# Performance work log

Measured on AMD Instinct MI355X. Metric: run time of the kernel, lower is better.

Reference implementation:

```python
import jax, jax.numpy as jnp
import numpy as np

N_EXPERTS = 8
D_MODEL = 1024
D_FF = 4096


def setup_inputs() -> dict:
    key = jax.random.key(0)
    k_x, k_idx, k_g, k_u, k_d = jax.random.split(key, 5)
    scale_in = 1.0 / np.sqrt(D_MODEL)
    scale_ff = 1.0 / np.sqrt(D_FF)
    return {
        "x": jax.random.normal(k_x, (2, 1024, D_MODEL), dtype=jnp.float32),
        "expert_idx": jax.random.randint(k_idx, (2, 1024), 0, N_EXPERTS, dtype=jnp.int64),
        "w_gate": jax.random.normal(k_g, (N_EXPERTS, D_MODEL, D_FF), dtype=jnp.float32) * scale_in,
        "w_up": jax.random.normal(k_u, (N_EXPERTS, D_MODEL, D_FF), dtype=jnp.float32) * scale_in,
        "w_down": jax.random.normal(k_d, (N_EXPERTS, D_FF, D_MODEL), dtype=jnp.float32) * scale_ff,
    }


def reference(x, expert_idx, w_gate, w_up, w_down):
    # x: [B, S, D]; expert_idx: [B, S] in [0, N_EXPERTS)
    B, S, D = x.shape
    x_flat = x.reshape(-1, D)                  # [T, D]
    idx_flat = expert_idx.reshape(-1)          # [T]
    out = jnp.zeros_like(x_flat)
    # Faithful per-expert dispatch: each token is processed by exactly one
    # expert's SwiGLU FFN; masked scatter-back combines results.
    for e in range(N_EXPERTS):
        mask = (idx_flat == e)[:, None]        # [T, 1]
        gate = jax.nn.silu(x_flat @ w_gate[e]) # [T, F]
        up = x_flat @ w_up[e]                  # [T, F]
        y = (gate * up) @ w_down[e]            # [T, D]
        out = jnp.where(mask, y, out)
    return out.reshape(B, S, D)
```

## Files before the change

kernel.cpp:

```cpp
#include <hip/hip_runtime.h>
#include <hip/hip_bf16.h>
#include <stdint.h>

#define N_EXPERTS 8
#define D_MODEL   1024
#define D_FF      4096
#define T_TOKENS  2048
#define MT1       128
#define MAXT1     24
#define MT2       64
#define MAXT2     40
#define BK        64
#define KP        72

typedef __attribute__((ext_vector_type(8))) short bf16x8;
typedef __attribute__((ext_vector_type(4))) float f32x4;

__device__ __forceinline__ short f2bf(float f) {
    union { float f; uint32_t u; } v; v.f = f;
    uint32_t u = v.u;
    return (short)((u + 0x7fffu + ((u >> 16) & 1u)) >> 16);
}

__device__ __forceinline__ uint32_t pack2bf(float a, float b) {
    __hip_bfloat162 h = __float22bfloat162_rn(make_float2(a, b));
    return *(uint32_t*)&h;
}

template<int STRIDE>
__device__ __forceinline__ void ldw16(float v[16], const float* __restrict__ src) {
#pragma unroll
    for (int j = 0; j < 16; ++j) v[j] = src[(size_t)j * STRIDE];
}

__device__ __forceinline__ void stw16(short* dst, const float v[16]) {
    uint4 w0, w1;
    w0.x = pack2bf(v[0], v[1]);  w0.y = pack2bf(v[2], v[3]);
    w0.z = pack2bf(v[4], v[5]);  w0.w = pack2bf(v[6], v[7]);
    w1.x = pack2bf(v[8], v[9]);  w1.y = pack2bf(v[10], v[11]);
    w1.z = pack2bf(v[12], v[13]); w1.w = pack2bf(v[14], v[15]);
    *(uint4*)dst = w0;
    *(uint4*)(dst + 8) = w1;
}


__global__ void moe_route(const int* __restrict__ idx, int* __restrict__ offsets,
                          int* __restrict__ nt1p, int* __restrict__ t1_e,
                          int* __restrict__ t1_p0, int* __restrict__ t1_end,
                          int* __restrict__ nt2p, int* __restrict__ t2_e,
                          int* __restrict__ t2_p0, int* __restrict__ t2_end) {
    __shared__ int cnt[N_EXPERTS];
    int tid = threadIdx.x;
    if (tid < N_EXPERTS) cnt[tid] = 0;
    __syncthreads();
    for (int t = tid; t < T_TOKENS; t += 256) atomicAdd(&cnt[idx[t]], 1);
    __syncthreads();
    if (tid == 0) {
        int off = 0, nt1 = 0, nt2 = 0;
        for (int e = 0; e < N_EXPERTS; ++e) {
            offsets[e] = off;
            int c = cnt[e], end = off + c;
            for (int i = 0; i < c; i += MT1) { t1_e[nt1] = e; t1_p0[nt1] = off + i; t1_end[nt1] = end; ++nt1; }
            for (int i = 0; i < c; i += MT2) { t2_e[nt2] = e; t2_p0[nt2] = off + i; t2_end[nt2] = end; ++nt2; }
            off = end;
        }
        offsets[N_EXPERTS] = off;
        *nt1p = nt1;
        *nt2p = nt2;
    }
}

__global__ void moe_gather(const float* __restrict__ x, const int* __restrict__ idx,
                           const int* __restrict__ offsets, int* __restrict__ cursor,
                           int* __restrict__ tok_of_row, short* __restrict__ Xg) {
    __shared__ int sp;
    int t = blockIdx.x;
    if (threadIdx.x == 0) {
        int e = idx[t];
        int p = offsets[e] + atomicAdd(&cursor[e], 1);
        tok_of_row[p] = t;
        sp = p;
    }
    __syncthreads();
    int p = sp;
    const float4* src = (const float4*)(x + (size_t)t * D_MODEL);
    uint2* dst = (uint2*)(Xg + (size_t)p * D_MODEL);
    int i = threadIdx.x;
    float4 v = src[i];
    uint2 o;
    o.x = pack2bf(v.x, v.y);
    o.y = pack2bf(v.z, v.w);
    dst[i] = o;
}


__launch_bounds__(256)
__global__ void moe_gemm1(const float* __restrict__ wg, const float* __restrict__ wu,
                          const short* __restrict__ Xg, short* __restrict__ h,
                          const int* __restrict__ tile_e, const int* __restrict__ tile_p0,
                          const int* __restrict__ tile_end, const int* __restrict__ ntiles) {
    int ti = blockIdx.y;
    if (ti >= *ntiles) return;
    int e = tile_e[ti], p0 = tile_p0[ti], pend = tile_end[ti];
    int n0 = blockIdx.x * 64;

    __shared__ short Bg[2][64][KP];
    __shared__ short Bu[2][64][KP];

    int tid = threadIdx.x;
    int nl = tid & 63, kc = tid >> 6;
    int lane = tid & 63, w = tid >> 6;
    int col = lane & 15, quad = lane >> 4;

    const float* wgb = wg + (size_t)e * D_MODEL * D_FF + (size_t)(kc * 16) * D_FF + n0 + nl;
    const float* wub = wu + (size_t)e * D_MODEL * D_FF + (size_t)(kc * 16) * D_FF + n0 + nl;

    int row0 = p0 + w * 32 + col;      if (row0 > T_TOKENS - 1) row0 = T_TOKENS - 1;
    int row1 = row0 + 16;              if (row1 > T_TOKENS - 1) row1 = T_TOKENS - 1;
    const short* a0p = Xg + (size_t)row0 * D_MODEL + quad * 8;
    const short* a1p = Xg + (size_t)row1 * D_MODEL + quad * 8;

    f32x4 accg[2][4], accu[2][4];
#pragma unroll
    for (int m = 0; m < 2; ++m)
#pragma unroll
        for (int nf = 0; nf < 4; ++nf) {
            accg[m][nf] = (f32x4){0,0,0,0};
            accu[m][nf] = (f32x4){0,0,0,0};
        }

    {
        float g0[16], u0[16];
        ldw16<D_FF>(g0, wgb);
        ldw16<D_FF>(u0, wub);
        stw16(&Bg[0][nl][kc * 16], g0);
        stw16(&Bu[0][nl][kc * 16], u0);
    }
    __syncthreads();

    bf16x8 a00 = *(const bf16x8*)(a0p);
    bf16x8 a01 = *(const bf16x8*)(a0p + 32);
    bf16x8 a10 = *(const bf16x8*)(a1p);
    bf16x8 a11 = *(const bf16x8*)(a1p + 32);

    const int NIT = D_MODEL / BK;
    int p = 0;
#pragma unroll 1
    for (int it = 0; it < NIT; ++it) {
        int kn = (it + 1 == NIT) ? 0 : (it + 1) * BK;
        float gn[16], un[16];
        ldw16<D_FF>(gn, wgb + (size_t)kn * D_FF);
        ldw16<D_FF>(un, wub + (size_t)kn * D_FF);
        bf16x8 a00n = *(const bf16x8*)(a0p + kn);
        bf16x8 a01n = *(const bf16x8*)(a0p + kn + 32);
        bf16x8 a10n = *(const bf16x8*)(a1p + kn);
        bf16x8 a11n = *(const bf16x8*)(a1p + kn + 32);

#pragma unroll
        for (int nf = 0; nf < 4; ++nf) {
            bf16x8 bg0 = *(const bf16x8*)&Bg[p][nf * 16 + col][quad * 8];
            bf16x8 bg1 = *(const bf16x8*)&Bg[p][nf * 16 + col][32 + quad * 8];
            bf16x8 bu0 = *(const bf16x8*)&Bu[p][nf * 16 + col][quad * 8];
            bf16x8 bu1 = *(const bf16x8*)&Bu[p][nf * 16 + col][32 + quad * 8];
            accg[0][nf] = __builtin_amdgcn_mfma_f32_16x16x32_bf16(a00, bg0, accg[0][nf], 0, 0, 0);
            accg[0][nf] = __builtin_amdgcn_mfma_f32_16x16x32_bf16(a01, bg1, accg[0][nf], 0, 0, 0);
            accg[1][nf] = __builtin_amdgcn_mfma_f32_16x16x32_bf16(a10, bg0, accg[1][nf], 0, 0, 0);
            accg[1][nf] = __builtin_amdgcn_mfma_f32_16x16x32_bf16(a11, bg1, accg[1][nf], 0, 0, 0);
            accu[0][nf] = __builtin_amdgcn_mfma_f32_16x16x32_bf16(a00, bu0, accu[0][nf], 0, 0, 0);
            accu[0][nf] = __builtin_amdgcn_mfma_f32_16x16x32_bf16(a01, bu1, accu[0][nf], 0, 0, 0);
            accu[1][nf] = __builtin_amdgcn_mfma_f32_16x16x32_bf16(a10, bu0, accu[1][nf], 0, 0, 0);
            accu[1][nf] = __builtin_amdgcn_mfma_f32_16x16x32_bf16(a11, bu1, accu[1][nf], 0, 0, 0);
        }

        stw16(&Bg[p ^ 1][nl][kc * 16], gn);
        stw16(&Bu[p ^ 1][nl][kc * 16], un);
        a00 = a00n; a01 = a01n; a10 = a10n; a11 = a11n;
        __syncthreads();
        p ^= 1;
    }

#pragma unroll
    for (int m = 0; m < 2; ++m) {
#pragma unroll
        for (int r = 0; r < 4; ++r) {
            int mr = p0 + w * 32 + m * 16 + quad * 4 + r;
            if (mr < pend) {
#pragma unroll
                for (int nf = 0; nf < 4; ++nf) {
                    float gv = accg[m][nf][r], uv = accu[m][nf][r];
                    float hv = (gv / (1.f + __expf(-gv))) * uv;
                    h[(size_t)mr * D_FF + n0 + nf * 16 + col] = f2bf(hv);
                }
            }
        }
    }
}


__launch_bounds__(256)
__global__ void moe_gemm2(const float* __restrict__ wd, const short* __restrict__ h,
                          const int* __restrict__ tok_of_row, float* __restrict__ out,
                          const int* __restrict__ tile_e, const int* __restrict__ tile_p0,
                          const int* __restrict__ tile_end, const int* __restrict__ ntiles) {
    int ti = blockIdx.y;
    if (ti >= *ntiles) return;
    int e = tile_e[ti], p0 = tile_p0[ti], pend = tile_end[ti];
    int d0 = blockIdx.x * 64;

    __shared__ short Bd[2][64][KP];

    int tid = threadIdx.x;
    int nl = tid & 63, kc = tid >> 6;
    int lane = tid & 63, w = tid >> 6;
    int col = lane & 15, quad = lane >> 4;

    const float* wb = wd + (size_t)e * D_FF * D_MODEL + (size_t)(kc * 16) * D_MODEL + d0 + nl;

    int row0 = p0 + w * 16 + col;      if (row0 > T_TOKENS - 1) row0 = T_TOKENS - 1;
    const short* a0p = h + (size_t)row0 * D_FF + quad * 8;

    f32x4 acc[4];
#pragma unroll
    for (int nf = 0; nf < 4; ++nf) acc[nf] = (f32x4){0,0,0,0};

    {
        float w0[16];
        ldw16<D_MODEL>(w0, wb);
        stw16(&Bd[0][nl][kc * 16], w0);
    }
    __syncthreads();

    bf16x8 a0 = *(const bf16x8*)(a0p);
    bf16x8 a1 = *(const bf16x8*)(a0p + 32);

    const int NIT = D_FF / BK;
    int p = 0;
#pragma unroll 1
    for (int it = 0; it < NIT; ++it) {
        int kn = (it + 1 == NIT) ? 0 : (it + 1) * BK;
        float wn[16];
        ldw16<D_MODEL>(wn, wb + (size_t)kn * D_MODEL);
        bf16x8 a0n = *(const bf16x8*)(a0p + kn);
        bf16x8 a1n = *(const bf16x8*)(a0p + kn + 32);

#pragma unroll
        for (int nf = 0; nf < 4; ++nf) {
            bf16x8 b0 = *(const bf16x8*)&Bd[p][nf * 16 + col][quad * 8];
            bf16x8 b1 = *(const bf16x8*)&Bd[p][nf * 16 + col][32 + quad * 8];
            acc[nf] = __builtin_amdgcn_mfma_f32_16x16x32_bf16(a0, b0, acc[nf], 0, 0, 0);
            acc[nf] = __builtin_amdgcn_mfma_f32_16x16x32_bf16(a1, b1, acc[nf], 0, 0, 0);
        }

        stw16(&Bd[p ^ 1][nl][kc * 16], wn);
        a0 = a0n; a1 = a1n;
        __syncthreads();
        p ^= 1;
    }

#pragma unroll
    for (int r = 0; r < 4; ++r) {
        int mr = p0 + w * 16 + quad * 4 + r;
        if (mr < pend) {
            int t = tok_of_row[mr];
#pragma unroll
            for (int nf = 0; nf < 4; ++nf)
                out[(size_t)t * D_MODEL + d0 + nf * 16 + col] = acc[nf][r];
        }
    }
}


extern "C" void kernel_launch(void* const* d_in, const int* in_sizes, int n_in,
                              void* d_out, int out_size, void* d_ws, size_t ws_size,
                              hipStream_t stream) {
    (void)in_sizes; (void)n_in; (void)out_size; (void)ws_size;
    const float* x   = (const float*)d_in[0];
    const int*   idx = (const int*)d_in[1];
    const float* wg  = (const float*)d_in[2];
    const float* wu  = (const float*)d_in[3];
    const float* wd  = (const float*)d_in[4];
    float* out = (float*)d_out;

    int* ws_i       = (int*)d_ws;
    int* cursor     = ws_i;
    int* offsets    = ws_i + 8;
    int* nt1        = ws_i + 20;
    int* nt2        = ws_i + 21;
    int* t1_e       = ws_i + 32;
    int* t1_p0      = ws_i + 56;
    int* t1_end     = ws_i + 80;
    int* t2_e       = ws_i + 104;
    int* t2_p0      = ws_i + 144;
    int* t2_end     = ws_i + 184;
    int* tok_of_row = ws_i + 256;

    short* Xg = (short*)((char*)d_ws + 16384);
    short* h  = (short*)((char*)d_ws + 16384 + (size_t)T_TOKENS * D_MODEL * 2);

    hipMemsetAsync(d_ws, 0, 128, stream);
    moe_route<<<dim3(1), 256, 0, stream>>>(idx, offsets, nt1, t1_e, t1_p0, t1_end,
                                           nt2, t2_e, t2_p0, t2_end);
    moe_gather<<<dim3(T_TOKENS), 256, 0, stream>>>(x, idx, offsets, cursor, tok_of_row, Xg);
    moe_gemm1<<<dim3(D_FF / 64, MAXT1), 256, 0, stream>>>(wg, wu, Xg, h,
                                                          t1_e, t1_p0, t1_end, nt1);
    moe_gemm2<<<dim3(D_MODEL / 64, MAXT2), 256, 0, stream>>>(wd, h, tok_of_row, out,
                                                             t2_e, t2_p0, t2_end, nt2);
}
```

Before: 506.7 us.

## Enlarge expert token tiles to 256 rows and split-K down projection with atomics

Raises the per-expert M tile from 128/64 rows to 256 rows in both GEMMs, so each fp32 weight tile is streamed and converted once per 256 tokens instead of per 128 or 64. This cuts repeated weight reads. The down-projection GEMM gains a 4-way K split, which keeps enough blocks in flight. Partial results are combined with float atomics into an output zeroed by a memset. The cost is larger per-thread accumulator register use, A operands loaded directly without prefetch, atomic traffic on the output, and nondeterministic summation order.

```diff
diff --git a/kernel.cpp b/kernel.cpp
--- a/kernel.cpp
+++ b/kernel.cpp
@@ -6,12 +6,12 @@
 #define D_MODEL   1024
 #define D_FF      4096
 #define T_TOKENS  2048
-#define MT1       128
-#define MAXT1     24
-#define MT2       64
-#define MAXT2     40
+#define MT        256
+#define MAXT      16
 #define BK        64
 #define KP        72
+#define KSPLIT    4
+#define KS2       (D_FF / KSPLIT)
 
 typedef __attribute__((ext_vector_type(8))) short bf16x8;
 typedef __attribute__((ext_vector_type(4))) float f32x4;
@@ -45,10 +45,8 @@
 
 
 __global__ void moe_route(const int* __restrict__ idx, int* __restrict__ offsets,
-                          int* __restrict__ nt1p, int* __restrict__ t1_e,
-                          int* __restrict__ t1_p0, int* __restrict__ t1_end,
-                          int* __restrict__ nt2p, int* __restrict__ t2_e,
-                          int* __restrict__ t2_p0, int* __restrict__ t2_end) {
+                          int* __restrict__ ntp, int* __restrict__ t_e,
+                          int* __restrict__ t_p0, int* __restrict__ t_end) {
     __shared__ int cnt[N_EXPERTS];
     int tid = threadIdx.x;
     if (tid < N_EXPERTS) cnt[tid] = 0;
@@ -56,17 +54,15 @@
     for (int t = tid; t < T_TOKENS; t += 256) atomicAdd(&cnt[idx[t]], 1);
     __syncthreads();
     if (tid == 0) {
-        int off = 0, nt1 = 0, nt2 = 0;
+        int off = 0, nt = 0;
         for (int e = 0; e < N_EXPERTS; ++e) {
             offsets[e] = off;
             int c = cnt[e], end = off + c;
-            for (int i = 0; i < c; i += MT1) { t1_e[nt1] = e; t1_p0[nt1] = off + i; t1_end[nt1] = end; ++nt1; }
-            for (int i = 0; i < c; i += MT2) { t2_e[nt2] = e; t2_p0[nt2] = off + i; t2_end[nt2] = end; ++nt2; }
+            for (int i = 0; i < c; i += MT) { t_e[nt] = e; t_p0[nt] = off + i; t_end[nt] = end; ++nt; }
             off = end;
         }
         offsets[N_EXPERTS] = off;
-        *nt1p = nt1;
-        *nt2p = nt2;
+        *ntp = nt;
     }
 }
 
@@ -94,7 +90,7 @@
 }
 
 
-__launch_bounds__(256)
+__launch_bounds__(256, 2)
 __global__ void moe_gemm1(const float* __restrict__ wg, const float* __restrict__ wu,
                           const short* __restrict__ Xg, short* __restrict__ h,
                           const int* __restrict__ tile_e, const int* __restrict__ tile_p0,
@@ -115,14 +111,17 @@
     const float* wgb = wg + (size_t)e * D_MODEL * D_FF + (size_t)(kc * 16) * D_FF + n0 + nl;
     const float* wub = wu + (size_t)e * D_MODEL * D_FF + (size_t)(kc * 16) * D_FF + n0 + nl;
 
-    int row0 = p0 + w * 32 + col;      if (row0 > T_TOKENS - 1) row0 = T_TOKENS - 1;
-    int row1 = row0 + 16;              if (row1 > T_TOKENS - 1) row1 = T_TOKENS - 1;
-    const short* a0p = Xg + (size_t)row0 * D_MODEL + quad * 8;
-    const short* a1p = Xg + (size_t)row1 * D_MODEL + quad * 8;
-
-    f32x4 accg[2][4], accu[2][4];
-#pragma unroll
-    for (int m = 0; m < 2; ++m)
+    const short* ap[4];
+#pragma unroll
+    for (int m = 0; m < 4; ++m) {
+        int row = p0 + w * 64 + m * 16 + col;
+        if (row > T_TOKENS - 1) row = T_TOKENS - 1;
+        ap[m] = Xg + (size_t)row * D_MODEL + quad * 8;
+    }
+
+    f32x4 accg[4][4], accu[4][4];
+#pragma unroll
+    for (int m = 0; m < 4; ++m)
 #pragma unroll
         for (int nf = 0; nf < 4; ++nf) {
             accg[m][nf] = (f32x4){0,0,0,0};
@@ -137,11 +136,6 @@
         stw16(&Bu[0][nl][kc * 16], u0);
     }
     __syncthreads();
-
-    bf16x8 a00 = *(const bf16x8*)(a0p);
-    bf16x8 a01 = *(const bf16x8*)(a0p + 32);
-    bf16x8 a10 = *(const bf16x8*)(a1p);
-    bf16x8 a11 = *(const bf16x8*)(a1p + 32);
 
     const int NIT = D_MODEL / BK;
     int p = 0;
@@ -151,39 +145,36 @@
         float gn[16], un[16];
         ldw16<D_FF>(gn, wgb + (size_t)kn * D_FF);
         ldw16<D_FF>(un, wub + (size_t)kn * D_FF);
-        bf16x8 a00n = *(const bf16x8*)(a0p + kn);
-        bf16x8 a01n = *(const bf16x8*)(a0p + kn + 32);
-        bf16x8 a10n = *(const bf16x8*)(a1p + kn);
-        bf16x8 a11n = *(const bf16x8*)(a1p + kn + 32);
-
-#pragma unroll
-        for (int nf = 0; nf < 4; ++nf) {
-            bf16x8 bg0 = *(const bf16x8*)&Bg[p][nf * 16 + col][quad * 8];
-            bf16x8 bg1 = *(const bf16x8*)&Bg[p][nf * 16 + col][32 + quad * 8];
-            bf16x8 bu0 = *(const bf16x8*)&Bu[p][nf * 16 + col][quad * 8];
-            bf16x8 bu1 = *(const bf16x8*)&Bu[p][nf * 16 + col][32 + quad * 8];
-            accg[0][nf] = __builtin_amdgcn_mfma_f32_16x16x32_bf16(a00, bg0, accg[0][nf], 0, 0, 0);
-            accg[0][nf] = __builtin_amdgcn_mfma_f32_16x16x32_bf16(a01, bg1, accg[0][nf], 0, 0, 0);
-            accg[1][nf] = __builtin_amdgcn_mfma_f32_16x16x32_bf16(a10, bg0, accg[1][nf], 0, 0, 0);
-            accg[1][nf] = __builtin_amdgcn_mfma_f32_16x16x32_bf16(a11, bg1, accg[1][nf], 0, 0, 0);
-            accu[0][nf] = __builtin_amdgcn_mfma_f32_16x16x32_bf16(a00, bu0, accu[0][nf], 0, 0, 0);
-            accu[0][nf] = __builtin_amdgcn_mfma_f32_16x16x32_bf16(a01, bu1, accu[0][nf], 0, 0, 0);
-            accu[1][nf] = __builtin_amdgcn_mfma_f32_16x16x32_bf16(a10, bu0, accu[1][nf], 0, 0, 0);
-            accu[1][nf] = __builtin_amdgcn_mfma_f32_16x16x32_bf16(a11, bu1, accu[1][nf], 0, 0, 0);
+        int kb = it * BK;
+
+#pragma unroll
+        for (int kk = 0; kk < 2; ++kk) {
+            bf16x8 am[4];
+#pragma unroll
+            for (int m = 0; m < 4; ++m) am[m] = *(const bf16x8*)(ap[m] + kb + kk * 32);
+#pragma unroll
+            for (int nf = 0; nf < 4; ++nf) {
+                bf16x8 bg = *(const bf16x8*)&Bg[p][nf * 16 + col][kk * 32 + quad * 8];
+                bf16x8 bu = *(const bf16x8*)&Bu[p][nf * 16 + col][kk * 32 + quad * 8];
+#pragma unroll
+                for (int m = 0; m < 4; ++m) {
+                    accg[m][nf] = __builtin_amdgcn_mfma_f32_16x16x32_bf16(am[m], bg, accg[m][nf], 0, 0, 0);
+                    accu[m][nf] = __builtin_amdgcn_mfma_f32_16x16x32_bf16(am[m], bu, accu[m][nf], 0, 0, 0);
+                }
+            }
         }
 
         stw16(&Bg[p ^ 1][nl][kc * 16], gn);
         stw16(&Bu[p ^ 1][nl][kc * 16], un);
-        a00 = a00n; a01 = a01n; a10 = a10n; a11 = a11n;
         __syncthreads();
         p ^= 1;
     }
 
 #pragma unroll
-    for (int m = 0; m < 2; ++m) {
+    for (int m = 0; m < 4; ++m) {
 #pragma unroll
         for (int r = 0; r < 4; ++r) {
-            int mr = p0 + w * 32 + m * 16 + quad * 4 + r;
+            int mr = p0 + w * 64 + m * 16 + quad * 4 + r;
             if (mr < pend) {
 #pragma unroll
                 for (int nf = 0; nf < 4; ++nf) {
@@ -197,7 +188,7 @@
 }
 
 
-__launch_bounds__(256)
+__launch_bounds__(256, 2)
 __global__ void moe_gemm2(const float* __restrict__ wd, const short* __restrict__ h,
                           const int* __restrict__ tok_of_row, float* __restrict__ out,
                           const int* __restrict__ tile_e, const int* __restrict__ tile_p0,
@@ -206,6 +197,7 @@
     if (ti >= *ntiles) return;
     int e = tile_e[ti], p0 = tile_p0[ti], pend = tile_end[ti];
     int d0 = blockIdx.x * 64;
+    int koff = blockIdx.z * KS2;
 
     __shared__ short Bd[2][64][KP];
 
@@ -214,14 +206,21 @@
     int lane = tid & 63, w = tid >> 6;
     int col = lane & 15, quad = lane >> 4;
 
-    const float* wb = wd + (size_t)e * D_FF * D_MODEL + (size_t)(kc * 16) * D_MODEL + d0 + nl;
-
-    int row0 = p0 + w * 16 + col;      if (row0 > T_TOKENS - 1) row0 = T_TOKENS - 1;
-    const short* a0p = h + (size_t)row0 * D_FF + quad * 8;
-
-    f32x4 acc[4];
-#pragma unroll
-    for (int nf = 0; nf < 4; ++nf) acc[nf] = (f32x4){0,0,0,0};
+    const float* wb = wd + (size_t)e * D_FF * D_MODEL + (size_t)(koff + kc * 16) * D_MODEL + d0 + nl;
+
+    const short* ap[4];
+#pragma unroll
+    for (int m = 0; m < 4; ++m) {
+        int row = p0 + w * 64 + m * 16 + col;
+        if (row > T_TOKENS - 1) row = T_TOKENS - 1;
+        ap[m] = h + (size_t)row * D_FF + koff + quad * 8;
+    }
+
+    f32x4 acc[4][4];
+#pragma unroll
+    for (int m = 0; m < 4; ++m)
+#pragma unroll
+        for (int nf = 0; nf < 4; ++nf) acc[m][nf] = (f32x4){0,0,0,0};
 
     {
         float w0[16];
@@ -230,41 +229,45 @@
     }
     __syncthreads();
 
-    bf16x8 a0 = *(const bf16x8*)(a0p);
-    bf16x8 a1 = *(const bf16x8*)(a0p + 32);
-
-    const int NIT = D_FF / BK;
+    const int NIT = KS2 / BK;
     int p = 0;
 #pragma unroll 1
     for (int it = 0; it < NIT; ++it) {
         int kn = (it + 1 == NIT) ? 0 : (it + 1) * BK;
         float wn[16];
         ldw16<D_MODEL>(wn, wb + (size_t)kn * D_MODEL);
-        bf16x8 a0n = *(const bf16x8*)(a0p + kn);
-        bf16x8 a1n = *(const bf16x8*)(a0p + kn + 32);
-
-#pragma unroll
-        for (int nf = 0; nf < 4; ++nf) {
-            bf16x8 b0 = *(const bf16x8*)&Bd[p][nf * 16 + col][quad * 8];
-            bf16x8 b1 = *(const bf16x8*)&Bd[p][nf * 16 + col][32 + quad * 8];
-            acc[nf] = __builtin_amdgcn_mfma_f32_16x16x32_bf16(a0, b0, acc[nf], 0, 0, 0);
-            acc[nf] = __builtin_amdgcn_mfma_f32_16x16x32_bf16(a1, b1, acc[nf], 0, 0, 0);
+        int kb = it * BK;
+
+#pragma unroll
+        for (int kk = 0; kk < 2; ++kk) {
+            bf16x8 am[4];
+#pragma unroll
+            for (int m = 0; m < 4; ++m) am[m] = *(const bf16x8*)(ap[m] + kb + kk * 32);
+#pragma unroll
+            for (int nf = 0; nf < 4; ++nf) {
+                bf16x8 b = *(const bf16x8*)&Bd[p][nf * 16 + col][kk * 32 + quad * 8];
+#pragma unroll
+                for (int m = 0; m < 4; ++m)
+                    acc[m][nf] = __builtin_amdgcn_mfma_f32_16x16x32_bf16(am[m], b, acc[m][nf], 0, 0, 0);
+            }
         }
 
         stw16(&Bd[p ^ 1][nl][kc * 16], wn);
-        a0 = a0n; a1 = a1n;
         __syncthreads();
         p ^= 1;
     }
 
 #pragma unroll
-    for (int r = 0; r < 4; ++r) {
-        int mr = p0 + w * 16 + quad * 4 + r;
-        if (mr < pend) {
-            int t = tok_of_row[mr];
-#pragma unroll
-            for (int nf = 0; nf < 4; ++nf)
-                out[(size_t)t * D_MODEL + d0 + nf * 16 + col] = acc[nf][r];
+    for (int m = 0; m < 4; ++m) {
+#pragma unroll
+        for (int r = 0; r < 4; ++r) {
+            int mr = p0 + w * 64 + m * 16 + quad * 4 + r;
+            if (mr < pend) {
+                int t = tok_of_row[mr];
+#pragma unroll
+                for (int nf = 0; nf < 4; ++nf)
+                    atomicAdd(&out[(size_t)t * D_MODEL + d0 + nf * 16 + col], acc[m][nf][r]);
+            }
         }
     }
 }
@@ -273,7 +276,7 @@
 extern "C" void kernel_launch(void* const* d_in, const int* in_sizes, int n_in,
                               void* d_out, int out_size, void* d_ws, size_t ws_size,
                               hipStream_t stream) {
-    (void)in_sizes; (void)n_in; (void)out_size; (void)ws_size;
+    (void)in_sizes; (void)n_in; (void)ws_size;
     const float* x   = (const float*)d_in[0];
     const int*   idx = (const int*)d_in[1];
     const float* wg  = (const float*)d_in[2];
@@ -284,25 +287,21 @@
     int* ws_i       = (int*)d_ws;
     int* cursor     = ws_i;
     int* offsets    = ws_i + 8;
-    int* nt1        = ws_i + 20;
-    int* nt2        = ws_i + 21;
-    int* t1_e       = ws_i + 32;
-    int* t1_p0      = ws_i + 56;
-    int* t1_end     = ws_i + 80;
-    int* t2_e       = ws_i + 104;
-    int* t2_p0      = ws_i + 144;
-    int* t2_end     = ws_i + 184;
-    int* tok_of_row = ws_i + 256;
+    int* nt         = ws_i + 20;
+    int* t_e        = ws_i + 32;
+    int* t_p0       = ws_i + 48;
+    int* t_end      = ws_i + 64;
+    int* tok_of_row = ws_i + 128;
 
     short* Xg = (short*)((char*)d_ws + 16384);
     short* h  = (short*)((char*)d_ws + 16384 + (size_t)T_TOKENS * D_MODEL * 2);
 
     hipMemsetAsync(d_ws, 0, 128, stream);
-    moe_route<<<dim3(1), 256, 0, stream>>>(idx, offsets, nt1, t1_e, t1_p0, t1_end,
-                                           nt2, t2_e, t2_p0, t2_end);
+    hipMemsetAsync(d_out, 0, (size_t)out_size * 4, stream);
+    moe_route<<<dim3(1), 256, 0, stream>>>(idx, offsets, nt, t_e, t_p0, t_end);
     moe_gather<<<dim3(T_TOKENS), 256, 0, stream>>>(x, idx, offsets, cursor, tok_of_row, Xg);
-    moe_gemm1<<<dim3(D_FF / 64, MAXT1), 256, 0, stream>>>(wg, wu, Xg, h,
-                                                          t1_e, t1_p0, t1_end, nt1);
-    moe_gemm2<<<dim3(D_MODEL / 64, MAXT2), 256, 0, stream>>>(wd, h, tok_of_row, out,
-                                                             t2_e, t2_p0, t2_end, nt2);
-}
+    moe_gemm1<<<dim3(D_FF / 64, MAXT), 256, 0, stream>>>(wg, wu, Xg, h,
+                                                         t_e, t_p0, t_end, nt);
+    moe_gemm2<<<dim3(D_MODEL / 64, MAXT, KSPLIT), 256, 0, stream>>>(wd, h, tok_of_row, out,
+                                                                    t_e, t_p0, t_end, nt);
+}
```

After: 563.8 us. 11.3% more time.
